# Kernel tuning notes

Measured on AMD Instinct MI355X. Metric: run time of the kernel, lower is better.

## Reference

```python
import jax, jax.numpy as jnp
import numpy as np

B, S, H = 32, 4096, 512

def setup_inputs() -> dict:
    key = jax.random.key(0)
    k1, k2, k3 = jax.random.split(key, 3)
    enc_output = jax.random.normal(k1, (B, S, H), dtype=jnp.float32)
    dec_output = jax.random.normal(k2, (B, 1, H), dtype=jnp.float32)
    # nn.Linear(H, H, bias=False) weight, applied as x @ W.T
    W = jax.random.normal(k3, (H, H), dtype=jnp.float32) * (1.0 / np.sqrt(H))
    return {"enc_output": enc_output, "dec_output": dec_output, "W": W}

def reference(enc_output, dec_output, W):
    # query = linear(dec_output.squeeze(1))  -> [B, H]
    query = jnp.einsum('bh,oh->bo', dec_output[:, 0, :], W)
    # scores = bmm(enc_output, query[..., None]).squeeze(-1) -> [B, S]
    scores = jnp.einsum('bsh,bh->bs', enc_output, query)
    # NOTE: original stores softmax(scores) in self.weight but uses the
    # RAW (pre-softmax) scores for the context bmm; reproduced faithfully.
    # context = bmm(scores[:, None, :], enc_output) -> [B, 1, H]
    context = jnp.einsum('bs,bsh->bh', scores, enc_output)[:, None, :]
    return context
```

## Files before the change

kernel.cpp:

```cpp
#include <hip/hip_runtime.h>

#define BB 32
#define SS 4096
#define HH 512

typedef float f4 __attribute__((ext_vector_type(4)));

__global__ __launch_bounds__(256) void query_kernel(const float* __restrict__ dec,
                                                    const float* __restrict__ W,
                                                    float* __restrict__ q) {
    const int gwave = (blockIdx.x * 256 + threadIdx.x) >> 6;
    const int lane  = threadIdx.x & 63;
    const int b = gwave >> 9;
    const int o = gwave & 511;

    const f4* wrow = (const f4*)(W  + (size_t)o * HH);
    const f4* drow = (const f4*)(dec + (size_t)b * HH);

    f4 w0 = wrow[lane], w1 = wrow[64 + lane];
    f4 d0 = drow[lane], d1 = drow[64 + lane];

    float s = w0.x*d0.x + w0.y*d0.y + w0.z*d0.z + w0.w*d0.w
            + w1.x*d1.x + w1.y*d1.y + w1.z*d1.z + w1.w*d1.w;

    #pragma unroll
    for (int off = 32; off >= 1; off >>= 1)
        s += __shfl_down(s, off, 64);

    if (lane == 0) q[gwave] = s;
}

__global__ __launch_bounds__(256) void fused_kernel(const float* __restrict__ enc,
                                                    const float* __restrict__ q,
                                                    float* __restrict__ out) {
    const int lane = threadIdx.x & 63;
    const int wave = threadIdx.x >> 6;
    const int b     = blockIdx.x >> 6;
    const int chunk = blockIdx.x & 63;

    const f4* q4 = (const f4*)(q + (size_t)b * HH);
    const f4 q0 = q4[lane];
    const f4 q1 = q4[64 + lane];

    f4 acc0 = {0.f, 0.f, 0.f, 0.f};
    f4 acc1 = {0.f, 0.f, 0.f, 0.f};

    const int rowBase = chunk * 64 + wave * 16;
    const f4* encBase = (const f4*)(enc + ((size_t)b * SS + rowBase) * HH);

    for (int rb = 0; rb < 16; rb += 4) {
        f4 e0[4], e1[4];
        #pragma unroll
        for (int r = 0; r < 4; ++r) {
            const f4* erow = encBase + (size_t)(rb + r) * 128;
            e0[r] = __builtin_nontemporal_load(erow + lane);
            e1[r] = __builtin_nontemporal_load(erow + 64 + lane);
        }

        float dot[4];
        #pragma unroll
        for (int r = 0; r < 4; ++r)
            dot[r] = e0[r].x*q0.x + e0[r].y*q0.y + e0[r].z*q0.z + e0[r].w*q0.w
                   + e1[r].x*q1.x + e1[r].y*q1.y + e1[r].z*q1.z + e1[r].w*q1.w;

        #pragma unroll
        for (int off = 1; off < 64; off <<= 1) {
            #pragma unroll
            for (int r = 0; r < 4; ++r)
                dot[r] += __shfl_xor(dot[r], off, 64);
        }

        #pragma unroll
        for (int r = 0; r < 4; ++r) {
            acc0.x += dot[r] * e0[r].x; acc0.y += dot[r] * e0[r].y;
            acc0.z += dot[r] * e0[r].z; acc0.w += dot[r] * e0[r].w;
            acc1.x += dot[r] * e1[r].x; acc1.y += dot[r] * e1[r].y;
            acc1.z += dot[r] * e1[r].z; acc1.w += dot[r] * e1[r].w;
        }
    }

    __shared__ float cbuf[4][HH];
    float* cw = cbuf[wave];
    ((f4*)(cw))[lane]       = acc0;
    ((f4*)(cw + 256))[lane] = acc1;
    __syncthreads();

    for (int c = threadIdx.x; c < HH; c += 256) {
        float v = cbuf[0][c] + cbuf[1][c] + cbuf[2][c] + cbuf[3][c];
        atomicAdd(out + (size_t)b * HH + c, v);
    }
}

extern "C" void kernel_launch(void* const* d_in, const int* in_sizes, int n_in,
                              void* d_out, int out_size, void* d_ws, size_t ws_size,
                              hipStream_t stream) {
    const float* enc = (const float*)d_in[0];
    const float* dec = (const float*)d_in[1];
    const float* W   = (const float*)d_in[2];
    float* out = (float*)d_out;
    float* q   = (float*)d_ws;

    (void)hipMemsetAsync(d_out, 0, (size_t)BB * HH * sizeof(float), stream);

    query_kernel<<<dim3(4096), dim3(256), 0, stream>>>(dec, W, q);

    fused_kernel<<<dim3(2048), dim3(256), 0, stream>>>(enc, q, out);
}
```

Baseline: 342.7 us.

## Split waves into 16-lane row groups and replace atomics with a partial-sum reduce kernel

The main kernel now has each wave process four rows at once, one per 16-lane group, so the dot-product reduction needs only four shuffle steps instead of six. Per-block results go to a workspace partial buffer, and a new reduce kernel sums them per batch, replacing the memset and global atomicAdds. The query kernel uses the same 16-lane grouping to compute four outputs per wave with a quarter of the blocks. In exchange there is an extra kernel launch, partial-buffer traffic, and more accumulator registers per lane.

```diff
diff --git a/kernel.cpp b/kernel.cpp
--- a/kernel.cpp
+++ b/kernel.cpp
@@ -9,86 +9,121 @@
 __global__ __launch_bounds__(256) void query_kernel(const float* __restrict__ dec,
                                                     const float* __restrict__ W,
                                                     float* __restrict__ q) {
-    const int gwave = (blockIdx.x * 256 + threadIdx.x) >> 6;
-    const int lane  = threadIdx.x & 63;
-    const int b = gwave >> 9;
-    const int o = gwave & 511;
+    const int wid  = (blockIdx.x * 256 + threadIdx.x) >> 6;
+    const int lane = threadIdx.x & 63;
+    const int l    = lane & 15;
+    const int g    = lane >> 4;
+    const int b  = wid >> 7;
+    const int o0 = (wid & 127) << 2;
 
-    const f4* wrow = (const f4*)(W  + (size_t)o * HH);
     const f4* drow = (const f4*)(dec + (size_t)b * HH);
+    const f4* wrow = (const f4*)(W + (size_t)(o0 + g) * HH);
 
-    f4 w0 = wrow[lane], w1 = wrow[64 + lane];
-    f4 d0 = drow[lane], d1 = drow[64 + lane];
+    float s = 0.f;
+    #pragma unroll
+    for (int k = 0; k < 8; ++k) {
+        f4 d = drow[l + 16 * k];
+        f4 w = wrow[l + 16 * k];
+        s += w.x * d.x + w.y * d.y + w.z * d.z + w.w * d.w;
+    }
+    s += __shfl_xor(s, 1, 64);
+    s += __shfl_xor(s, 2, 64);
+    s += __shfl_xor(s, 4, 64);
+    s += __shfl_xor(s, 8, 64);
 
-    float s = w0.x*d0.x + w0.y*d0.y + w0.z*d0.z + w0.w*d0.w
-            + w1.x*d1.x + w1.y*d1.y + w1.z*d1.z + w1.w*d1.w;
-
-    #pragma unroll
-    for (int off = 32; off >= 1; off >>= 1)
-        s += __shfl_down(s, off, 64);
-
-    if (lane == 0) q[gwave] = s;
+    if (l == 0) q[(size_t)b * HH + o0 + g] = s;
 }
 
 __global__ __launch_bounds__(256) void fused_kernel(const float* __restrict__ enc,
                                                     const float* __restrict__ q,
-                                                    float* __restrict__ out) {
+                                                    float* __restrict__ partial) {
     const int lane = threadIdx.x & 63;
     const int wave = threadIdx.x >> 6;
+    const int l    = lane & 15;
+    const int g    = lane >> 4;
     const int b     = blockIdx.x >> 6;
     const int chunk = blockIdx.x & 63;
 
     const f4* q4 = (const f4*)(q + (size_t)b * HH);
-    const f4 q0 = q4[lane];
-    const f4 q1 = q4[64 + lane];
+    f4 qr[8];
+    #pragma unroll
+    for (int k = 0; k < 8; ++k) qr[k] = q4[l + 16 * k];
 
-    f4 acc0 = {0.f, 0.f, 0.f, 0.f};
-    f4 acc1 = {0.f, 0.f, 0.f, 0.f};
+    f4 acc[8];
+    #pragma unroll
+    for (int k = 0; k < 8; ++k) acc[k] = {0.f, 0.f, 0.f, 0.f};
 
     const int rowBase = chunk * 64 + wave * 16;
     const f4* encBase = (const f4*)(enc + ((size_t)b * SS + rowBase) * HH);
 
-    for (int rb = 0; rb < 16; rb += 4) {
-        f4 e0[4], e1[4];
+    for (int set = 0; set < 4; ++set) {
+        const f4* rp = encBase + (size_t)(set * 4 + g) * 128;
+        f4 e[8];
         #pragma unroll
-        for (int r = 0; r < 4; ++r) {
-            const f4* erow = encBase + (size_t)(rb + r) * 128;
-            e0[r] = __builtin_nontemporal_load(erow + lane);
-            e1[r] = __builtin_nontemporal_load(erow + 64 + lane);
-        }
+        for (int k = 0; k < 8; ++k)
+            e[k] = __builtin_nontemporal_load(rp + l + 16 * k);
 
-        float dot[4];
+        float dot = 0.f;
         #pragma unroll
-        for (int r = 0; r < 4; ++r)
-            dot[r] = e0[r].x*q0.x + e0[r].y*q0.y + e0[r].z*q0.z + e0[r].w*q0.w
-                   + e1[r].x*q1.x + e1[r].y*q1.y + e1[r].z*q1.z + e1[r].w*q1.w;
+        for (int k = 0; k < 8; ++k)
+            dot += e[k].x * qr[k].x + e[k].y * qr[k].y
+                 + e[k].z * qr[k].z + e[k].w * qr[k].w;
+
+        dot += __shfl_xor(dot, 1, 64);
+        dot += __shfl_xor(dot, 2, 64);
+        dot += __shfl_xor(dot, 4, 64);
+        dot += __shfl_xor(dot, 8, 64);
 
         #pragma unroll
-        for (int off = 1; off < 64; off <<= 1) {
-            #pragma unroll
-            for (int r = 0; r < 4; ++r)
-                dot[r] += __shfl_xor(dot[r], off, 64);
-        }
-
-        #pragma unroll
-        for (int r = 0; r < 4; ++r) {
-            acc0.x += dot[r] * e0[r].x; acc0.y += dot[r] * e0[r].y;
-            acc0.z += dot[r] * e0[r].z; acc0.w += dot[r] * e0[r].w;
-            acc1.x += dot[r] * e1[r].x; acc1.y += dot[r] * e1[r].y;
-            acc1.z += dot[r] * e1[r].z; acc1.w += dot[r] * e1[r].w;
+        for (int k = 0; k < 8; ++k) {
+            acc[k].x += dot * e[k].x;
+            acc[k].y += dot * e[k].y;
+            acc[k].z += dot * e[k].z;
+            acc[k].w += dot * e[k].w;
         }
     }
 
-    __shared__ float cbuf[4][HH];
-    float* cw = cbuf[wave];
-    ((f4*)(cw))[lane]       = acc0;
-    ((f4*)(cw + 256))[lane] = acc1;
+    #pragma unroll
+    for (int k = 0; k < 8; ++k) {
+        acc[k].x += __shfl_xor(acc[k].x, 16, 64);
+        acc[k].y += __shfl_xor(acc[k].y, 16, 64);
+        acc[k].z += __shfl_xor(acc[k].z, 16, 64);
+        acc[k].w += __shfl_xor(acc[k].w, 16, 64);
+        acc[k].x += __shfl_xor(acc[k].x, 32, 64);
+        acc[k].y += __shfl_xor(acc[k].y, 32, 64);
+        acc[k].z += __shfl_xor(acc[k].z, 32, 64);
+        acc[k].w += __shfl_xor(acc[k].w, 32, 64);
+    }
+
+    __shared__ f4 cbuf[4][128];
+    if (g == 0) {
+        #pragma unroll
+        for (int k = 0; k < 8; ++k) cbuf[wave][l + 16 * k] = acc[k];
+    }
     __syncthreads();
 
-    for (int c = threadIdx.x; c < HH; c += 256) {
-        float v = cbuf[0][c] + cbuf[1][c] + cbuf[2][c] + cbuf[3][c];
-        atomicAdd(out + (size_t)b * HH + c, v);
+    if (threadIdx.x < 128) {
+        f4 v = cbuf[0][threadIdx.x] + cbuf[1][threadIdx.x]
+             + cbuf[2][threadIdx.x] + cbuf[3][threadIdx.x];
+        ((f4*)(partial + (size_t)blockIdx.x * HH))[threadIdx.x] = v;
     }
+}
+
+__global__ __launch_bounds__(128) void reduce_kernel(const f4* __restrict__ partial,
+                                                     f4* __restrict__ out) {
+    const int b = blockIdx.x;
+    const int t = threadIdx.x;
+    const f4* p = partial + (size_t)b * 64 * 128 + t;
+
+    f4 v0 = {0.f, 0.f, 0.f, 0.f}, v1 = v0, v2 = v0, v3 = v0;
+    #pragma unroll 4
+    for (int j = 0; j < 64; j += 4) {
+        v0 += p[(size_t)(j + 0) * 128];
+        v1 += p[(size_t)(j + 1) * 128];
+        v2 += p[(size_t)(j + 2) * 128];
+        v3 += p[(size_t)(j + 3) * 128];
+    }
+    out[(size_t)b * 128 + t] = (v0 + v1) + (v2 + v3);
 }
 
 extern "C" void kernel_launch(void* const* d_in, const int* in_sizes, int n_in,
@@ -98,11 +133,13 @@
     const float* dec = (const float*)d_in[1];
     const float* W   = (const float*)d_in[2];
     float* out = (float*)d_out;
-    float* q   = (float*)d_ws;
+    float* q       = (float*)d_ws;
+    float* partial = (float*)d_ws + BB * HH;
 
-    (void)hipMemsetAsync(d_out, 0, (size_t)BB * HH * sizeof(float), stream);
 
-    query_kernel<<<dim3(4096), dim3(256), 0, stream>>>(dec, W, q);
+    query_kernel<<<dim3(1024), dim3(256), 0, stream>>>(dec, W, q);
 
-    fused_kernel<<<dim3(2048), dim3(256), 0, stream>>>(enc, q, out);
+    fused_kernel<<<dim3(2048), dim3(256), 0, stream>>>(enc, q, partial);
+
+    reduce_kernel<<<dim3(32), dim3(128), 0, stream>>>((const f4*)partial, (f4*)out);
 }
```

Result: no change. 342.3 us (-0.1%).
